# Optimization experiments

Measured on AMD Instinct MI355X. Metric: run time of the kernel, lower is better.

Reference implementation:

```python
import jax, jax.numpy as jnp
import numpy as np

N = 50000   # nodes
E = 800000  # edges (before self loops)
D_IN = 128
D_H = 128
C = 10
BN_EPS = 1e-5


def setup_inputs() -> dict:
    key = jax.random.key(0)
    ks = jax.random.split(key, 8)
    x = jax.random.normal(ks[0], (N, D_IN), dtype=jnp.float32)
    edge_index = jax.random.randint(ks[1], (2, E), 0, N, dtype=jnp.int32)
    s = 1.0 / np.sqrt(D_IN)  # ~xavier scale for square layers
    W1 = jax.random.normal(ks[2], (D_IN, D_H), dtype=jnp.float32) * s
    W2 = jax.random.normal(ks[3], (D_H, D_H), dtype=jnp.float32) * s
    W3 = jax.random.normal(ks[4], (D_H, D_H), dtype=jnp.float32) * s
    Wf = jax.random.normal(ks[5], (3 * D_H, C), dtype=jnp.float32) * (1.0 / np.sqrt(3 * D_H))
    zeros_h = jnp.zeros((D_H,), jnp.float32)
    ones_h = jnp.ones((D_H,), jnp.float32)
    return dict(
        x=x, edge_index=edge_index,
        W1=W1, b1=zeros_h, W2=W2, b2=zeros_h, W3=W3, b3=zeros_h,
        g1=ones_h, be1=zeros_h, g2=ones_h, be2=zeros_h, g3=ones_h, be3=zeros_h,
        Wf=Wf, bf=jnp.zeros((C,), jnp.float32),
    )


def _edges_with_norm(edge_index):
    # Add self loops, then symmetric GCN normalization: D^-1/2 (A+I) D^-1/2
    loop = jnp.arange(N, dtype=edge_index.dtype)
    row = jnp.concatenate([edge_index[0], loop])  # source
    col = jnp.concatenate([edge_index[1], loop])  # destination
    deg = jax.ops.segment_sum(jnp.ones_like(col, jnp.float32), col, num_segments=N)
    dinv = jnp.where(deg > 0, jax.lax.rsqrt(deg), 0.0)
    norm = dinv[row] * dinv[col]  # [E+N]
    return row, col, norm


def _gcn_conv(h, W, b, row, col, norm):
    h = h @ W  # linear first (as in PyG GCNConv)
    msg = h[row] * norm[:, None]           # gather + scale, [E+N, D]
    agg = jax.ops.segment_sum(msg, col, num_segments=N)  # scatter-add
    return agg + b


def _bn(h, g, b):
    # training-mode batch norm over the node dim (biased variance, as torch)
    m = h.mean(axis=0)
    v = jnp.mean((h - m) ** 2, axis=0)
    return g * (h - m) * jax.lax.rsqrt(v + BN_EPS) + b


def reference(x, edge_index, W1, b1, W2, b2, W3, b3,
              g1, be1, g2, be2, g3, be3, Wf, bf):
    row, col, norm = _edges_with_norm(edge_index)
    h1 = jax.nn.relu(_bn(_gcn_conv(x, W1, b1, row, col, norm), g1, be1))
    h2 = jax.nn.relu(_bn(_gcn_conv(h1, W2, b2, row, col, norm), g2, be2))
    h3 = jax.nn.relu(_bn(_gcn_conv(h2, W3, b3, row, col, norm), g3, be3))
    cat = jnp.concatenate([h1, h2, h3], axis=1)  # [N, 3*D_H]
    # dropout in eval mode == identity; identity readout (node level)
    return cat @ Wf + bf
```

## Files before the change

kernel.cpp:

```cpp
#include <hip/hip_runtime.h>

#define N_NODES 50000
#define N_EDGES 800000
#define D 128
#define C_OUT 10
#define BN_EPS 1e-5f
#define CAP 64
#define MTILE 32
#define GEMM_GRID 1563
#define LINKB 782
#define AGG_BLOCKS 2048
#define NCOPY 32
#define CSTR 136


typedef unsigned int uint32;
typedef __attribute__((ext_vector_type(8))) short bf16x8;
typedef __attribute__((ext_vector_type(4))) float f32x4;

__device__ __forceinline__ float bf2f(unsigned int u16) {
    unsigned int x = u16 << 16;
    float f;
    __builtin_memcpy(&f, &x, 4);
    return f;
}
__device__ __forceinline__ unsigned int f2bf(float f) {
    unsigned int x;
    __builtin_memcpy(&x, &f, 4);
    unsigned int r = x + 0x7FFFu + ((x >> 16) & 1u);
    return r >> 16;
}
__device__ __forceinline__ uint32 pack_bf2(float a, float b) {
    return f2bf(a) | (f2bf(b) << 16);
}


__global__ void k_setup(const float* __restrict__ W1, const float* __restrict__ W2,
                        const float* __restrict__ W3, const float* __restrict__ Wf,
                        unsigned short* __restrict__ WT, unsigned short* __restrict__ WfT,
                        int* __restrict__ cntp, float* __restrict__ sums) {
    int b = blockIdx.x, tid = threadIdx.x;
    if (b < 192) {
        int idx = b * 256 + tid;
        int mat = idx >> 14, rem = idx & 16383;
        int n = rem >> 7, k = rem & 127;
        const float* W = (mat == 0) ? W1 : ((mat == 1) ? W2 : W3);
        WT[idx] = (unsigned short)f2bf(W[k * 128 + n]);
    } else if (b < 216) {
        int idx = (b - 192) * 256 + tid;
        if (idx < 6144) {
            int li = idx >> 11, rem = idx & 2047;
            int n = rem >> 7, k = rem & 127;
            WfT[idx] = (n < C_OUT) ? (unsigned short)f2bf(Wf[(li * 128 + k) * C_OUT + n]) : 0;
        }
    } else {
        int i = (b - 216) * 256 + tid;
        if (i < N_NODES) cntp[i << 4] = 0;
        if (i < 3 * NCOPY * 256) sums[i] = 0.0f;
    }
}


__global__ void k_dinv(const int* __restrict__ cntp, int* __restrict__ cnt,
                       float* __restrict__ dinv) {
    int i = blockIdx.x * blockDim.x + threadIdx.x;
    if (i >= N_NODES) return;
    int c = cntp[i << 4];
    cnt[i] = (c < CAP) ? c : CAP;
    dinv[i] = rsqrtf((float)(c + 1));
}


__global__ void k_bnfin(const float* __restrict__ sums, const float* __restrict__ g,
                        const float* __restrict__ be, float* __restrict__ st) {
    int t = threadIdx.x;
    float sm = 0.f, sq = 0.f;
    for (int c = 0; c < NCOPY; ++c) {
        sm += sums[c * 256 + t];
        sq += sums[c * 256 + 128 + t];
    }
    float mean = sm * (1.0f / N_NODES);
    float var = fmaxf(sq * (1.0f / N_NODES) - mean * mean, 0.f);
    float s = g[t] * rsqrtf(var + BN_EPS);
    st[t] = s;
    st[128 + t] = be[t] - mean * s;
}


__global__ __launch_bounds__(128) void k_gemm(const float* __restrict__ Af32,
                                              const unsigned short* __restrict__ Abf,
                                              const unsigned short* __restrict__ WT,
                                              unsigned short* __restrict__ hl,
                                              const float* __restrict__ st,
                                              const unsigned short* __restrict__ WfT,
                                              const float* __restrict__ bfv,
                                              float* __restrict__ outp, int mode,
                                              const float* __restrict__ dinvp,
                                              const int* __restrict__ linkEi,
                                              int* __restrict__ cntp,
                                              int* __restrict__ adj) {
    __shared__ unsigned short SM[MTILE * CSTR];
    unsigned short* As = SM;
    int tid = threadIdx.x;
    int bid = blockIdx.x;

    if (linkEi && bid >= GEMM_GRID) {
        int lb = bid - GEMM_GRID;
        int d8[8], s8[8];
#pragma unroll
        for (int u = 0; u < 8; ++u) {
            int e = (lb * 8 + u) * 128 + tid;
            d8[u] = (e < N_EDGES) ? linkEi[N_EDGES + e] : -1;
            s8[u] = (e < N_EDGES) ? linkEi[e] : 0;
        }
#pragma unroll
        for (int u = 0; u < 8; ++u) {
            if (d8[u] >= 0) {
                int slot = atomicAdd(&cntp[d8[u] << 4], 1);
                if (slot < CAP) adj[(d8[u] << 6) + slot] = s8[u];
            }
        }
        return;
    }
    int row0 = bid * MTILE;

    if (Abf) {
        int c8 = tid & 15, cc = c8 * 8;
        float s8[8], t8[8];
        {
            float4 a0 = *(const float4*)&st[cc];
            float4 a1 = *(const float4*)&st[cc + 4];
            float4 b0 = *(const float4*)&st[128 + cc];
            float4 b1 = *(const float4*)&st[128 + cc + 4];
            s8[0] = a0.x; s8[1] = a0.y; s8[2] = a0.z; s8[3] = a0.w;
            s8[4] = a1.x; s8[5] = a1.y; s8[6] = a1.z; s8[7] = a1.w;
            t8[0] = b0.x; t8[1] = b0.y; t8[2] = b0.z; t8[3] = b0.w;
            t8[4] = b1.x; t8[5] = b1.y; t8[6] = b1.z; t8[7] = b1.w;
        }
        const uint4* H4 = (const uint4*)Abf;
#pragma unroll
        for (int i = 0; i < 4; ++i) {
            int idx = i * 128 + tid;
            int r = idx >> 4;
            int gr = row0 + r;
            uint4 v = make_uint4(0, 0, 0, 0);
            if (gr < N_NODES) v = H4[(size_t)gr * 16 + c8];
            uint32 w[4] = {v.x, v.y, v.z, v.w};
            uint32 o[4];
#pragma unroll
            for (int p = 0; p < 4; ++p) {
                float f0 = bf2f(w[p] & 0xFFFFu) * s8[2 * p] + t8[2 * p];
                float f1 = bf2f(w[p] >> 16) * s8[2 * p + 1] + t8[2 * p + 1];
                o[p] = pack_bf2(fmaxf(f0, 0.f), fmaxf(f1, 0.f));
            }
            int swz = c8 ^ (r & 15);
            *(uint4*)&As[r * 128 + swz * 8] = make_uint4(o[0], o[1], o[2], o[3]);
        }
    } else {
        const float4* A4 = (const float4*)Af32;
        int c4 = tid & 31;
#pragma unroll
        for (int i = 0; i < 8; ++i) {
            int idx = i * 128 + tid;
            int r = idx >> 5;
            int gr = row0 + r;
            float4 v = make_float4(0.f, 0.f, 0.f, 0.f);
            if (gr < N_NODES) v = A4[(size_t)gr * 32 + c4];
            ushort4 o;
            o.x = (unsigned short)f2bf(v.x);
            o.y = (unsigned short)f2bf(v.y);
            o.z = (unsigned short)f2bf(v.z);
            o.w = (unsigned short)f2bf(v.w);
            int swz = (c4 >> 1) ^ (r & 15);
            *(ushort4*)&As[r * 128 + swz * 8 + (c4 & 1) * 4] = o;
        }
    }
    __syncthreads();

    int wave = tid >> 6, lane = tid & 63;
    int quad = lane >> 4, l16 = lane & 15;
    int m0 = wave * 16;
    int m = m0 + l16;

    bf16x8 af[4];
#pragma unroll
    for (int ks = 0; ks < 4; ++ks) {
        int swz = (ks * 4 + quad) ^ (m & 15);
        af[ks] = *(bf16x8*)&As[m * 128 + swz * 8];
    }

    f32x4 acc[8];
#pragma unroll
    for (int nt = 0; nt < 8; ++nt) acc[nt] = (f32x4){0.f, 0.f, 0.f, 0.f};

#pragma unroll
    for (int nt = 0; nt < 8; ++nt) {
        int n = nt * 16 + l16;
        bf16x8 bfr[4];
#pragma unroll
        for (int ks = 0; ks < 4; ++ks)
            bfr[ks] = *(const bf16x8*)&WT[n * 128 + (ks * 4 + quad) * 8];
#pragma unroll
        for (int ks = 0; ks < 4; ++ks)
            acc[nt] = __builtin_amdgcn_mfma_f32_16x16x32_bf16(af[ks], bfr[ks], acc[nt], 0, 0, 0);
    }

    if (mode != 0) {
        f32x4 accO = (f32x4){0.f, 0.f, 0.f, 0.f};
#pragma unroll
        for (int ks = 0; ks < 4; ++ks) {
            bf16x8 bw = *(const bf16x8*)&WfT[l16 * 128 + (ks * 4 + quad) * 8];
            accO = __builtin_amdgcn_mfma_f32_16x16x32_bf16(af[ks], bw, accO, 0, 0, 0);
        }
        if (l16 < C_OUT) {
#pragma unroll
            for (int reg = 0; reg < 4; ++reg) {
                int gm = row0 + m0 + quad * 4 + reg;
                if (gm < N_NODES) {
                    size_t o = (size_t)gm * C_OUT + l16;
                    float v = accO[reg];
                    if (mode == 1) outp[o] = v + bfv[l16];
                    else outp[o] += v;
                }
            }
        }
    }

    float dv[4] = {1.f, 1.f, 1.f, 1.f};
    if (dinvp) {
#pragma unroll
        for (int reg = 0; reg < 4; ++reg) {
            int gm = row0 + m0 + quad * 4 + reg;
            dv[reg] = (gm < N_NODES) ? dinvp[gm] : 0.f;
        }
    }

    __syncthreads();
#pragma unroll
    for (int reg = 0; reg < 4; ++reg) {
        int lm = m0 + quad * 4 + reg;
#pragma unroll
        for (int nt = 0; nt < 8; ++nt)
            SM[lm * CSTR + nt * 16 + l16] = (unsigned short)f2bf(acc[nt][reg] * dv[reg]);
    }
    __syncthreads();
    uint4* H4o = (uint4*)hl;
#pragma unroll
    for (int i = 0; i < 4; ++i) {
        int idx = i * 128 + tid;
        int r = idx >> 4, c8 = idx & 15;
        int gr = row0 + r;
        if (gr < N_NODES)
            H4o[(size_t)gr * 16 + c8] = *(uint4*)&SM[r * CSTR + c8 * 8];
    }
}


__global__ __launch_bounds__(256) void k_agg(const unsigned short* __restrict__ hl,
                                             const int* __restrict__ adj,
                                             const int* __restrict__ cnt,
                                             const float* __restrict__ dinv,
                                             unsigned short* __restrict__ agg,
                                             float* __restrict__ sums,
                                             int scaled) {
    __shared__ float red[4][256];
    int tid = threadIdx.x;
    int lane = tid & 63;
    int gw = (blockIdx.x << 2) | (tid >> 6);
    float sx = 0.f, qx = 0.f, sy = 0.f, qy = 0.f;

    for (int node = gw; node < N_NODES; node += AGG_BLOCKS * 4) {
        const int* row = adj + ((size_t)node << 6);
        int n = cnt[node];
        float di = dinv[node];
        uint32 ps = *(const uint32*)&hl[(size_t)node * 128 + lane * 2];
        float ax, ay;
        if (scaled) {
            ax = bf2f(ps & 0xFFFFu);
            ay = bf2f(ps >> 16);
        } else {
            ax = bf2f(ps & 0xFFFFu) * di;
            ay = bf2f(ps >> 16) * di;
        }
        int e = 0;
        for (; e + 7 < n; e += 8) {
            int j[8];
#pragma unroll
            for (int u = 0; u < 8; ++u) j[u] = row[e + u];
            uint32 p[8];
#pragma unroll
            for (int u = 0; u < 8; ++u)
                p[u] = *(const uint32*)&hl[(size_t)j[u] * 128 + lane * 2];
            if (scaled) {
#pragma unroll
                for (int u = 0; u < 8; ++u) {
                    ax += bf2f(p[u] & 0xFFFFu);
                    ay += bf2f(p[u] >> 16);
                }
            } else {
                float w[8];
#pragma unroll
                for (int u = 0; u < 8; ++u) w[u] = dinv[j[u]];
#pragma unroll
                for (int u = 0; u < 8; ++u) {
                    ax += bf2f(p[u] & 0xFFFFu) * w[u];
                    ay += bf2f(p[u] >> 16) * w[u];
                }
            }
        }
        for (; e < n; ++e) {
            int j = row[e];
            uint32 p = *(const uint32*)&hl[(size_t)j * 128 + lane * 2];
            if (scaled) {
                ax += bf2f(p & 0xFFFFu);
                ay += bf2f(p >> 16);
            } else {
                float w = dinv[j];
                ax += bf2f(p & 0xFFFFu) * w;
                ay += bf2f(p >> 16) * w;
            }
        }
        float ox = ax * di, oy = ay * di;
        *(uint32*)&agg[(size_t)node * 128 + lane * 2] = pack_bf2(ox, oy);
        sx += ox; qx += ox * ox; sy += oy; qy += oy * oy;
    }

    red[0][tid] = sx; red[1][tid] = qx; red[2][tid] = sy; red[3][tid] = qy;
    __syncthreads();
    int s = tid >> 6, l = tid & 63;
    float v = red[s][l] + red[s][64 + l] + red[s][128 + l] + red[s][192 + l];
    atomicAdd(&sums[((blockIdx.x & (NCOPY - 1)) << 8) + (s & 1) * 128 + 2 * l + (s >> 1)], v);
}


__global__ __launch_bounds__(128) void k_out_mfma(const unsigned short* __restrict__ h,
                                                  const unsigned short* __restrict__ WfT,
                                                  float* __restrict__ outp,
                                                  const float* __restrict__ st) {
    __shared__ unsigned short As[MTILE * 128];
    int tid = threadIdx.x;
    int row0 = blockIdx.x * MTILE;

    int c8 = tid & 15, cc = c8 * 8;
    float s8[8], t8[8];
    {
        float4 a0 = *(const float4*)&st[cc];
        float4 a1 = *(const float4*)&st[cc + 4];
        float4 b0 = *(const float4*)&st[128 + cc];
        float4 b1 = *(const float4*)&st[128 + cc + 4];
        s8[0] = a0.x; s8[1] = a0.y; s8[2] = a0.z; s8[3] = a0.w;
        s8[4] = a1.x; s8[5] = a1.y; s8[6] = a1.z; s8[7] = a1.w;
        t8[0] = b0.x; t8[1] = b0.y; t8[2] = b0.z; t8[3] = b0.w;
        t8[4] = b1.x; t8[5] = b1.y; t8[6] = b1.z; t8[7] = b1.w;
    }
    const uint4* H4 = (const uint4*)h;
#pragma unroll
    for (int i = 0; i < 4; ++i) {
        int idx = i * 128 + tid;
        int r = idx >> 4;
        int gr = row0 + r;
        uint4 v = make_uint4(0, 0, 0, 0);
        if (gr < N_NODES) v = H4[(size_t)gr * 16 + c8];
        uint32 w[4] = {v.x, v.y, v.z, v.w};
        uint32 o[4];
#pragma unroll
        for (int p = 0; p < 4; ++p) {
            float f0 = bf2f(w[p] & 0xFFFFu) * s8[2 * p] + t8[2 * p];
            float f1 = bf2f(w[p] >> 16) * s8[2 * p + 1] + t8[2 * p + 1];
            o[p] = pack_bf2(fmaxf(f0, 0.f), fmaxf(f1, 0.f));
        }
        int swz = c8 ^ (r & 15);
        *(uint4*)&As[r * 128 + swz * 8] = make_uint4(o[0], o[1], o[2], o[3]);
    }
    __syncthreads();

    int wave = tid >> 6, lane = tid & 63;
    int quad = lane >> 4, l16 = lane & 15;
    int m0 = wave * 16;
    int m = m0 + l16;

    f32x4 accO = (f32x4){0.f, 0.f, 0.f, 0.f};
#pragma unroll
    for (int ks = 0; ks < 4; ++ks) {
        bf16x8 bw = *(const bf16x8*)&WfT[l16 * 128 + (ks * 4 + quad) * 8];
        int swz = (ks * 4 + quad) ^ (m & 15);
        bf16x8 av = *(bf16x8*)&As[m * 128 + swz * 8];
        accO = __builtin_amdgcn_mfma_f32_16x16x32_bf16(av, bw, accO, 0, 0, 0);
    }
    if (l16 < C_OUT) {
#pragma unroll
        for (int reg = 0; reg < 4; ++reg) {
            int gm = row0 + m0 + quad * 4 + reg;
            if (gm < N_NODES)
                outp[(size_t)gm * C_OUT + l16] += accO[reg];
        }
    }
}


extern "C" void kernel_launch(void* const* d_in, const int* in_sizes, int n_in,
                              void* d_out, int out_size, void* d_ws, size_t ws_size,
                              hipStream_t stream) {
    const float* x  = (const float*)d_in[0];
    const int*   ei = (const int*)d_in[1];
    const float* W1 = (const float*)d_in[2];
    const float* W2 = (const float*)d_in[4];
    const float* W3 = (const float*)d_in[6];
    const float* g1  = (const float*)d_in[8];
    const float* be1 = (const float*)d_in[9];
    const float* g2  = (const float*)d_in[10];
    const float* be2 = (const float*)d_in[11];
    const float* g3  = (const float*)d_in[12];
    const float* be3 = (const float*)d_in[13];
    const float* Wf  = (const float*)d_in[14];
    const float* bf  = (const float*)d_in[15];
    float* out = (float*)d_out;

    char* ws = (char*)d_ws;
    size_t off = 0;
    auto alloc = [&](size_t bytes) -> void* {
        void* p = ws + off;
        off = (off + bytes + 255) & ~(size_t)255;
        return p;
    };
    int*   cntp  = (int*)alloc((size_t)N_NODES * 16 * 4);
    int*   adj   = (int*)alloc((size_t)N_NODES * CAP * 4);
    int*   cnt   = (int*)alloc((size_t)N_NODES * 4);
    float* dinv  = (float*)alloc((size_t)N_NODES * 4);
    float* sums  = (float*)alloc((size_t)3 * NCOPY * 256 * 4);
    float* st    = (float*)alloc((size_t)3 * 256 * 4);
    unsigned short* WT   = (unsigned short*)alloc((size_t)3 * 128 * 128 * 2);
    unsigned short* WfT  = (unsigned short*)alloc((size_t)3 * 16 * 128 * 2);
    unsigned short* hl   = (unsigned short*)alloc((size_t)N_NODES * 128 * 2);
    unsigned short* bufA = (unsigned short*)alloc((size_t)N_NODES * 128 * 2);
    unsigned short* bufB = (unsigned short*)alloc((size_t)N_NODES * 128 * 2);

    const int TPB = 256;
    const int SL = NCOPY * 256;
    k_setup<<<412, 256, 0, stream>>>(W1, W2, W3, Wf, WT, WfT, cntp, sums);

    k_gemm<<<GEMM_GRID + LINKB, 128, 0, stream>>>(
        x, nullptr, WT, hl, nullptr, nullptr,
        nullptr, nullptr, 0, nullptr, ei, cntp, adj);
    k_dinv<<<(N_NODES + TPB - 1) / TPB, TPB, 0, stream>>>(cntp, cnt, dinv);
    k_agg<<<AGG_BLOCKS, 256, 0, stream>>>(hl, adj, cnt, dinv, bufA, sums + 0, 0);
    k_bnfin<<<1, 128, 0, stream>>>(sums + 0, g1, be1, st + 0);

    k_gemm<<<GEMM_GRID, 128, 0, stream>>>(nullptr, bufA, WT + 16384, hl, st + 0,
                                          WfT, bf, out, 1, dinv, nullptr, nullptr, nullptr);
    k_agg<<<AGG_BLOCKS, 256, 0, stream>>>(hl, adj, cnt, dinv, bufB, sums + SL, 1);
    k_bnfin<<<1, 128, 0, stream>>>(sums + SL, g2, be2, st + 256);

    k_gemm<<<GEMM_GRID, 128, 0, stream>>>(nullptr, bufB, WT + 32768, hl, st + 256,
                                          WfT + 2048, nullptr, out, 2, dinv,
                                          nullptr, nullptr, nullptr);
    k_agg<<<AGG_BLOCKS, 256, 0, stream>>>(hl, adj, cnt, dinv, bufA, sums + 2 * SL, 1);
    k_bnfin<<<1, 128, 0, stream>>>(sums + 2 * SL, g3, be3, st + 512);

    k_out_mfma<<<GEMM_GRID, 128, 0, stream>>>(bufA, WfT + 4096, out, st + 512);
}
```

Baseline: 397.6 us.

## Halve GEMM row tile, split columns across waves, and specialize aggregation kernels

The fused GEMM now processes 16 rows per block instead of 32, so it launches twice as many blocks. Its two waves now split the 128 output columns between them rather than splitting rows, and only wave 0 computes the classifier partial. The output kernel keeps a separate 32-row tile. The aggregation kernel is split into a weighted first-layer version and an unweighted later-layer version, which removes the runtime `scaled` branch and interleaves the `dinv` loads with the feature gathers. The aim is more parallelism in the GEMM stage and a leaner aggregation loop, at the cost of less reuse of the weight loads per block.

```diff
diff --git a/kernel.cpp b/kernel.cpp
--- a/kernel.cpp
+++ b/kernel.cpp
@@ -6,8 +6,10 @@
 #define C_OUT 10
 #define BN_EPS 1e-5f
 #define CAP 64
-#define MTILE 32
-#define GEMM_GRID 1563
+#define MTILE 16
+#define GEMM_GRID 3125
+#define OTILE 32
+#define OUT_GRID 1563
 #define LINKB 782
 #define AGG_BLOCKS 2048
 #define NCOPY 32
@@ -139,9 +141,8 @@
         }
         const uint4* H4 = (const uint4*)Abf;
 #pragma unroll
-        for (int i = 0; i < 4; ++i) {
-            int idx = i * 128 + tid;
-            int r = idx >> 4;
+        for (int i = 0; i < 2; ++i) {
+            int r = i * 8 + (tid >> 4);
             int gr = row0 + r;
             uint4 v = make_uint4(0, 0, 0, 0);
             if (gr < N_NODES) v = H4[(size_t)gr * 16 + c8];
@@ -160,9 +161,8 @@
         const float4* A4 = (const float4*)Af32;
         int c4 = tid & 31;
 #pragma unroll
-        for (int i = 0; i < 8; ++i) {
-            int idx = i * 128 + tid;
-            int r = idx >> 5;
+        for (int i = 0; i < 4; ++i) {
+            int r = i * 4 + (tid >> 5);
             int gr = row0 + r;
             float4 v = make_float4(0.f, 0.f, 0.f, 0.f);
             if (gr < N_NODES) v = A4[(size_t)gr * 32 + c4];
@@ -179,23 +179,22 @@
 
     int wave = tid >> 6, lane = tid & 63;
     int quad = lane >> 4, l16 = lane & 15;
-    int m0 = wave * 16;
-    int m = m0 + l16;
+    int m = l16;
 
     bf16x8 af[4];
 #pragma unroll
     for (int ks = 0; ks < 4; ++ks) {
-        int swz = (ks * 4 + quad) ^ (m & 15);
+        int swz = (ks * 4 + quad) ^ l16;
         af[ks] = *(bf16x8*)&As[m * 128 + swz * 8];
     }
 
-    f32x4 acc[8];
-#pragma unroll
-    for (int nt = 0; nt < 8; ++nt) acc[nt] = (f32x4){0.f, 0.f, 0.f, 0.f};
-
-#pragma unroll
-    for (int nt = 0; nt < 8; ++nt) {
-        int n = nt * 16 + l16;
+    f32x4 acc[4];
+#pragma unroll
+    for (int nt = 0; nt < 4; ++nt) acc[nt] = (f32x4){0.f, 0.f, 0.f, 0.f};
+
+#pragma unroll
+    for (int nt = 0; nt < 4; ++nt) {
+        int n = (wave * 4 + nt) * 16 + l16;
         bf16x8 bfr[4];
 #pragma unroll
         for (int ks = 0; ks < 4; ++ks)
@@ -205,7 +204,7 @@
             acc[nt] = __builtin_amdgcn_mfma_f32_16x16x32_bf16(af[ks], bfr[ks], acc[nt], 0, 0, 0);
     }
 
-    if (mode != 0) {
+    if (mode != 0 && wave == 0) {
         f32x4 accO = (f32x4){0.f, 0.f, 0.f, 0.f};
 #pragma unroll
         for (int ks = 0; ks < 4; ++ks) {
@@ -215,7 +214,7 @@
         if (l16 < C_OUT) {
 #pragma unroll
             for (int reg = 0; reg < 4; ++reg) {
-                int gm = row0 + m0 + quad * 4 + reg;
+                int gm = row0 + quad * 4 + reg;
                 if (gm < N_NODES) {
                     size_t o = (size_t)gm * C_OUT + l16;
                     float v = accO[reg];
@@ -230,7 +229,7 @@
     if (dinvp) {
 #pragma unroll
         for (int reg = 0; reg < 4; ++reg) {
-            int gm = row0 + m0 + quad * 4 + reg;
+            int gm = row0 + quad * 4 + reg;
             dv[reg] = (gm < N_NODES) ? dinvp[gm] : 0.f;
         }
     }
@@ -238,17 +237,17 @@
     __syncthreads();
 #pragma unroll
     for (int reg = 0; reg < 4; ++reg) {
-        int lm = m0 + quad * 4 + reg;
-#pragma unroll
-        for (int nt = 0; nt < 8; ++nt)
-            SM[lm * CSTR + nt * 16 + l16] = (unsigned short)f2bf(acc[nt][reg] * dv[reg]);
+        int lm = quad * 4 + reg;
+#pragma unroll
+        for (int nt = 0; nt < 4; ++nt)
+            SM[lm * CSTR + (wave * 4 + nt) * 16 + l16] =
+                (unsigned short)f2bf(acc[nt][reg] * dv[reg]);
     }
     __syncthreads();
     uint4* H4o = (uint4*)hl;
 #pragma unroll
-    for (int i = 0; i < 4; ++i) {
-        int idx = i * 128 + tid;
-        int r = idx >> 4, c8 = idx & 15;
+    for (int i = 0; i < 2; ++i) {
+        int r = i * 8 + (tid >> 4), c8 = tid & 15;
         int gr = row0 + r;
         if (gr < N_NODES)
             H4o[(size_t)gr * 16 + c8] = *(uint4*)&SM[r * CSTR + c8 * 8];
@@ -256,13 +255,12 @@
 }
 
 
-__global__ __launch_bounds__(256) void k_agg(const unsigned short* __restrict__ hl,
-                                             const int* __restrict__ adj,
-                                             const int* __restrict__ cnt,
-                                             const float* __restrict__ dinv,
-                                             unsigned short* __restrict__ agg,
-                                             float* __restrict__ sums,
-                                             int scaled) {
+__global__ __launch_bounds__(256) void k_agg0(const unsigned short* __restrict__ hl,
+                                              const int* __restrict__ adj,
+                                              const int* __restrict__ cnt,
+                                              const float* __restrict__ dinv,
+                                              unsigned short* __restrict__ agg,
+                                              float* __restrict__ sums) {
     __shared__ float red[4][256];
     int tid = threadIdx.x;
     int lane = tid & 63;
@@ -274,51 +272,85 @@
         int n = cnt[node];
         float di = dinv[node];
         uint32 ps = *(const uint32*)&hl[(size_t)node * 128 + lane * 2];
-        float ax, ay;
-        if (scaled) {
-            ax = bf2f(ps & 0xFFFFu);
-            ay = bf2f(ps >> 16);
-        } else {
-            ax = bf2f(ps & 0xFFFFu) * di;
-            ay = bf2f(ps >> 16) * di;
-        }
+        float ax = bf2f(ps & 0xFFFFu) * di;
+        float ay = bf2f(ps >> 16) * di;
         int e = 0;
         for (; e + 7 < n; e += 8) {
             int j[8];
 #pragma unroll
             for (int u = 0; u < 8; ++u) j[u] = row[e + u];
+            float w[8];
+            uint32 p[8];
+#pragma unroll
+            for (int u = 0; u < 8; ++u) {
+                w[u] = dinv[j[u]];
+                p[u] = *(const uint32*)&hl[(size_t)j[u] * 128 + lane * 2];
+            }
+#pragma unroll
+            for (int u = 0; u < 8; ++u) {
+                ax += bf2f(p[u] & 0xFFFFu) * w[u];
+                ay += bf2f(p[u] >> 16) * w[u];
+            }
+        }
+        for (; e < n; ++e) {
+            int j = row[e];
+            float w = dinv[j];
+            uint32 p = *(const uint32*)&hl[(size_t)j * 128 + lane * 2];
+            ax += bf2f(p & 0xFFFFu) * w;
+            ay += bf2f(p >> 16) * w;
+        }
+        float ox = ax * di, oy = ay * di;
+        *(uint32*)&agg[(size_t)node * 128 + lane * 2] = pack_bf2(ox, oy);
+        sx += ox; qx += ox * ox; sy += oy; qy += oy * oy;
+    }
+
+    red[0][tid] = sx; red[1][tid] = qx; red[2][tid] = sy; red[3][tid] = qy;
+    __syncthreads();
+    int s = tid >> 6, l = tid & 63;
+    float v = red[s][l] + red[s][64 + l] + red[s][128 + l] + red[s][192 + l];
+    atomicAdd(&sums[((blockIdx.x & (NCOPY - 1)) << 8) + (s & 1) * 128 + 2 * l + (s >> 1)], v);
+}
+
+
+__global__ __launch_bounds__(256) void k_agg1(const unsigned short* __restrict__ hl,
+                                              const int* __restrict__ adj,
+                                              const int* __restrict__ cnt,
+                                              const float* __restrict__ dinv,
+                                              unsigned short* __restrict__ agg,
+                                              float* __restrict__ sums) {
+    __shared__ float red[4][256];
+    int tid = threadIdx.x;
+    int lane = tid & 63;
+    int gw = (blockIdx.x << 2) | (tid >> 6);
+    float sx = 0.f, qx = 0.f, sy = 0.f, qy = 0.f;
+
+    for (int node = gw; node < N_NODES; node += AGG_BLOCKS * 4) {
+        const int* row = adj + ((size_t)node << 6);
+        int n = cnt[node];
+        float di = dinv[node];
+        uint32 ps = *(const uint32*)&hl[(size_t)node * 128 + lane * 2];
+        float ax = bf2f(ps & 0xFFFFu);
+        float ay = bf2f(ps >> 16);
+        int e = 0;
+        for (; e + 7 < n; e += 8) {
+            int j[8];
+#pragma unroll
+            for (int u = 0; u < 8; ++u) j[u] = row[e + u];
             uint32 p[8];
 #pragma unroll
             for (int u = 0; u < 8; ++u)
                 p[u] = *(const uint32*)&hl[(size_t)j[u] * 128 + lane * 2];
-            if (scaled) {
-#pragma unroll
-                for (int u = 0; u < 8; ++u) {
-                    ax += bf2f(p[u] & 0xFFFFu);
-                    ay += bf2f(p[u] >> 16);
-                }
-            } else {
-                float w[8];
-#pragma unroll
-                for (int u = 0; u < 8; ++u) w[u] = dinv[j[u]];
-#pragma unroll
-                for (int u = 0; u < 8; ++u) {
-                    ax += bf2f(p[u] & 0xFFFFu) * w[u];
-                    ay += bf2f(p[u] >> 16) * w[u];
-                }
+#pragma unroll
+            for (int u = 0; u < 8; ++u) {
+                ax += bf2f(p[u] & 0xFFFFu);
+                ay += bf2f(p[u] >> 16);
             }
         }
         for (; e < n; ++e) {
             int j = row[e];
             uint32 p = *(const uint32*)&hl[(size_t)j * 128 + lane * 2];
-            if (scaled) {
-                ax += bf2f(p & 0xFFFFu);
-                ay += bf2f(p >> 16);
-            } else {
-                float w = dinv[j];
-                ax += bf2f(p & 0xFFFFu) * w;
-                ay += bf2f(p >> 16) * w;
-            }
+            ax += bf2f(p & 0xFFFFu);
+            ay += bf2f(p >> 16);
         }
         float ox = ax * di, oy = ay * di;
         *(uint32*)&agg[(size_t)node * 128 + lane * 2] = pack_bf2(ox, oy);
@@ -337,9 +369,9 @@
                                                   const unsigned short* __restrict__ WfT,
                                                   float* __restrict__ outp,
                                                   const float* __restrict__ st) {
-    __shared__ unsigned short As[MTILE * 128];
+    __shared__ unsigned short As[OTILE * 128];
     int tid = threadIdx.x;
-    int row0 = blockIdx.x * MTILE;
+    int row0 = blockIdx.x * OTILE;
 
     int c8 = tid & 15, cc = c8 * 8;
     float s8[8], t8[8];
@@ -443,19 +475,19 @@
         x, nullptr, WT, hl, nullptr, nullptr,
         nullptr, nullptr, 0, nullptr, ei, cntp, adj);
     k_dinv<<<(N_NODES + TPB - 1) / TPB, TPB, 0, stream>>>(cntp, cnt, dinv);
-    k_agg<<<AGG_BLOCKS, 256, 0, stream>>>(hl, adj, cnt, dinv, bufA, sums + 0, 0);
+    k_agg0<<<AGG_BLOCKS, 256, 0, stream>>>(hl, adj, cnt, dinv, bufA, sums + 0);
     k_bnfin<<<1, 128, 0, stream>>>(sums + 0, g1, be1, st + 0);
 
     k_gemm<<<GEMM_GRID, 128, 0, stream>>>(nullptr, bufA, WT + 16384, hl, st + 0,
                                           WfT, bf, out, 1, dinv, nullptr, nullptr, nullptr);
-    k_agg<<<AGG_BLOCKS, 256, 0, stream>>>(hl, adj, cnt, dinv, bufB, sums + SL, 1);
+    k_agg1<<<AGG_BLOCKS, 256, 0, stream>>>(hl, adj, cnt, dinv, bufB, sums + SL);
     k_bnfin<<<1, 128, 0, stream>>>(sums + SL, g2, be2, st + 256);
 
     k_gemm<<<GEMM_GRID, 128, 0, stream>>>(nullptr, bufB, WT + 32768, hl, st + 256,
                                           WfT + 2048, nullptr, out, 2, dinv,
                                           nullptr, nullptr, nullptr);
-    k_agg<<<AGG_BLOCKS, 256, 0, stream>>>(hl, adj, cnt, dinv, bufA, sums + 2 * SL, 1);
+    k_agg1<<<AGG_BLOCKS, 256, 0, stream>>>(hl, adj, cnt, dinv, bufA, sums + 2 * SL);
     k_bnfin<<<1, 128, 0, stream>>>(sums + 2 * SL, g3, be3, st + 512);
 
-    k_out_mfma<<<GEMM_GRID, 128, 0, stream>>>(bufA, WfT + 4096, out, st + 512);
-}
+    k_out_mfma<<<OUT_GRID, 128, 0, stream>>>(bufA, WfT + 4096, out, st + 512);
+}
```

Result: faster. 333.1 us (-16.2%).
